# Kernel tuning notes

Measured on AMD Instinct MI355X. Metric: run time of the kernel, lower is better.

## Reference

```python
import jax, jax.numpy as jnp
import numpy as np

S, B, D_MODEL, H = 2048, 2, 1024, 16
DH = D_MODEL // H
SCALE = 1.0 / np.sqrt(DH)
NEG_INF = jnp.float32(-1e30)


def setup_inputs() -> dict:
    key = jax.random.key(0)
    ks = jax.random.split(key, 12)
    std = 1.0 / np.sqrt(D_MODEL)
    inp = {
        "query": jax.random.normal(ks[0], (S, B, D_MODEL), jnp.float32),
        "key": jax.random.normal(ks[1], (S, B, D_MODEL), jnp.float32),
        "value": jax.random.normal(ks[2], (S, B, D_MODEL), jnp.float32),
        # causal mask, shape (seq_q, seq_k, 1) per prepare_mask asserts
        "mask": jnp.tril(jnp.ones((S, S), dtype=bool))[:, :, None],
        # params stored (in, out) for x @ W
        "Wq": jax.random.normal(ks[3], (D_MODEL, H * DH), jnp.float32) * std,
        "bq": jnp.zeros((H * DH,), jnp.float32),
        "Wk": jax.random.normal(ks[4], (D_MODEL, H * DH), jnp.float32) * std,
        "bk": jnp.zeros((H * DH,), jnp.float32),
        "Wv": jax.random.normal(ks[5], (D_MODEL, H * DH), jnp.float32) * std,
        "bv": jnp.zeros((H * DH,), jnp.float32),
        "Wo": jax.random.normal(ks[6], (D_MODEL, D_MODEL), jnp.float32) * std,
        "bo": jnp.zeros((D_MODEL,), jnp.float32),
    }
    return inp


def reference(query, key, value, mask, Wq, bq, Wk, bk, Wv, bv, Wo, bo):
    seq_len, batch, _ = query.shape
    # project and split heads: (S, B, H, DH)
    q = (query @ Wq + bq).reshape(seq_len, batch, H, DH)
    k = (key @ Wk + bk).reshape(key.shape[0], batch, H, DH)
    v = (value @ Wv + bv).reshape(value.shape[0], batch, H, DH)
    # scores: (seq_q, batch, heads, seq_k)
    scores = jnp.einsum("ibhd,jbhd->ibhj", q, k) * SCALE
    # mask (seq_q, seq_k, batch_or_1) -> broadcast to (seq_q, batch, 1, seq_k)
    m = jnp.transpose(mask, (0, 2, 1))[:, :, None, :]
    scores = jnp.where(m, scores, NEG_INF)
    attn = jax.nn.softmax(scores, axis=-1)  # dropout_prob=0.0 (eval)
    x = jnp.einsum("ibhj,jbhd->ibhd", attn, v)
    x = x.reshape(seq_len, batch, H * DH)
    return x @ Wo + bo
```

## Files before the change

kernel.cpp:

```cpp
#include <hip/hip_runtime.h>
#include <hip/hip_bf16.h>
#include <cstdint>

#define S_LEN 2048
#define BATCH 2
#define DM    1024
#define NH    16
#define DH    64

typedef short s8v __attribute__((ext_vector_type(8)));
typedef float f4v __attribute__((ext_vector_type(4)));
typedef unsigned int u32x2 __attribute__((ext_vector_type(2)));

__device__ __forceinline__ ushort f2bf(float x) {
  union { float f; uint32_t u; } v; v.f = x;
  uint32_t r = v.u + 0x7fffu + ((v.u >> 16) & 1u);
  return (ushort)(r >> 16);
}
__device__ __forceinline__ float bf2f(ushort u) {
  union { uint32_t u; float f; } v; v.u = (uint32_t)u << 16; return v.f;
}
__device__ __forceinline__ uint32_t fbits(float x) {
  union { float f; uint32_t u; } v; v.f = x; return v.u;
}
__device__ __forceinline__ uint32_t bfrnd(uint32_t u) {
  return u + 0x7fffu + ((u >> 16) & 1u);
}
__device__ __forceinline__ uint32_t packbf(uint32_t flo, uint32_t fhi) {
  return __builtin_amdgcn_perm(bfrnd(fhi), bfrnd(flo), 0x07060302u);
}
__device__ __forceinline__ uint32_t packbf_tr(float lo, float hi) {
  return __builtin_amdgcn_perm(fbits(hi), fbits(lo), 0x07060302u);
}

typedef __attribute__((address_space(1))) const void gas_void;
typedef __attribute__((address_space(3))) void las_void;
__device__ __forceinline__ void gld16(void* l, const void* g) {
  __builtin_amdgcn_global_load_lds((gas_void*)(uintptr_t)g,
                                   (las_void*)(uintptr_t)l, 16, 0, 0);
}

__global__ __launch_bounds__(256)
void prep(const float* W0, const float* W1, const float* W2, const float* W3,
          ushort* T0, ushort* T1, ushort* T2, ushort* T3,
          const float* X0, const float* X1, const float* X2,
          ushort* O0, ushort* O1, ushort* O2) {
  const int z = blockIdx.z;
  if (z < 4) {
    if (blockIdx.x >= 1024) return;
    const float* W = z == 0 ? W0 : z == 1 ? W1 : z == 2 ? W2 : W3;
    ushort*      T = z == 0 ? T0 : z == 1 ? T1 : z == 2 ? T2 : T3;
    __shared__ ushort tile[32][33];
    const int n0 = (blockIdx.x & 31) * 32, k0 = (blockIdx.x >> 5) * 32;
    const int tx = threadIdx.x & 31, ty = threadIdx.x >> 5;
    #pragma unroll
    for (int r = ty; r < 32; r += 8)
      tile[r][tx] = f2bf(W[(size_t)(k0 + r) * DM + n0 + tx]);
    __syncthreads();
    #pragma unroll
    for (int r = ty; r < 32; r += 8)
      T[(size_t)(n0 + r) * DM + k0 + tx] = tile[tx][r];
  } else {
    const float* X = z == 4 ? X0 : z == 5 ? X1 : X2;
    ushort*      O = z == 4 ? O0 : z == 5 ? O1 : O2;
    const size_t i = ((size_t)blockIdx.x * 256 + threadIdx.x) * 4;
    const float4 v = *(const float4*)(X + i);
    ushort4 h;
    h.x = f2bf(v.x); h.y = f2bf(v.y); h.z = f2bf(v.z); h.w = f2bf(v.w);
    *(ushort4*)(O + i) = h;
  }
}

__global__ __launch_bounds__(512, 2)
void gemm_qkv(const ushort* __restrict__ Xq, const ushort* __restrict__ Xk,
              const ushort* __restrict__ Xv,
              const ushort* __restrict__ Wqt, const ushort* __restrict__ Wkt,
              const ushort* __restrict__ Wvt,
              const float* __restrict__ bq, const float* __restrict__ bk,
              const float* __restrict__ bv,
              ushort* __restrict__ Qh, ushort* __restrict__ Kh,
              ushort* __restrict__ Vt) {
  const int z = blockIdx.z;
  const ushort* A    = z == 0 ? Xq  : z == 1 ? Xk  : Xv;
  const ushort* Bt   = z == 0 ? Wqt : z == 1 ? Wkt : Wvt;
  const float*  bias = z == 0 ? bq  : z == 1 ? bk  : bv;

  __shared__ __align__(16) ushort lds[65536];

  const int tid = threadIdx.x, lane = tid & 63, w = tid >> 6;
  const int wm = w >> 2, wn = w & 3;
  const int lrow = lane & 15, quad = lane >> 4;
  const int m0 = blockIdx.x * 256, n0 = blockIdx.y * 256;

  const int tr = tid >> 2;
  const int swz = ((tid & 3) ^ ((tid >> 3) & 3)) * 8;
  const ushort* gA0 = A  + (size_t)(m0 + tr) * DM + swz;
  const ushort* gA1 = A  + (size_t)(m0 + 128 + tr) * DM + swz;
  const ushort* gB0 = Bt + (size_t)(n0 + tr) * DM + swz;
  const ushort* gB1 = Bt + (size_t)(n0 + 128 + tr) * DM + swz;
  const int dA0 = w * 512, dA1 = 4096 + w * 512;
  const int dB0 = 8192 + w * 512, dB1 = 12288 + w * 512;

  const int fr = (lrow >> 1) & 3;
  int pa[8], pb[4];
  #pragma unroll
  for (int i = 0; i < 8; i++)
    pa[i] = (wm * 128 + i * 16 + lrow) * 32 + ((quad ^ fr) * 8);
  #pragma unroll
  for (int j = 0; j < 4; j++)
    pb[j] = 8192 + (wn * 64 + j * 16 + lrow) * 32 + ((quad ^ fr) * 8);

  f4v acc[8][4];
  #pragma unroll
  for (int i = 0; i < 8; i++)
    #pragma unroll
    for (int j = 0; j < 4; j++)
      acc[i][j] = f4v{0.f, 0.f, 0.f, 0.f};

  #pragma unroll
  for (int t = 0; t < 3; t++) {
    const int bb = t * 16384, ko = t * 32;
    gld16(&lds[bb + dA0], gA0 + ko);
    gld16(&lds[bb + dA1], gA1 + ko);
    gld16(&lds[bb + dB0], gB0 + ko);
    gld16(&lds[bb + dB1], gB1 + ko);
  }
  asm volatile("s_waitcnt vmcnt(8)" ::: "memory");
  __builtin_amdgcn_s_barrier();

  for (int t = 0; t < 32; t++) {
    const int bb = (t & 3) * 16384;
    const bool st = t < 29;
    const int sbb = ((t + 3) & 3) * 16384;
    const int ko = (t + 3) * 32;
    s8v af[4], bf[4];
    #pragma unroll
    for (int i = 0; i < 4; i++) af[i] = *(const s8v*)&lds[bb + pa[i]];
    #pragma unroll
    for (int j = 0; j < 4; j++) bf[j] = *(const s8v*)&lds[bb + pb[j]];
    if (st) { gld16(&lds[sbb + dA0], gA0 + ko); gld16(&lds[sbb + dA1], gA1 + ko); }
    __builtin_amdgcn_s_barrier();
    __builtin_amdgcn_s_setprio(1);
    #pragma unroll
    for (int i = 0; i < 4; i++)
      #pragma unroll
      for (int j = 0; j < 4; j++)
        acc[i][j] = __builtin_amdgcn_mfma_f32_16x16x32_bf16(af[i], bf[j], acc[i][j], 0, 0, 0);
    __builtin_amdgcn_s_setprio(0);
    __builtin_amdgcn_s_barrier();
    #pragma unroll
    for (int i = 0; i < 4; i++) af[i] = *(const s8v*)&lds[bb + pa[4 + i]];
    if (st) { gld16(&lds[sbb + dB0], gB0 + ko); gld16(&lds[sbb + dB1], gB1 + ko); }
    __builtin_amdgcn_s_barrier();
    __builtin_amdgcn_s_setprio(1);
    #pragma unroll
    for (int i = 0; i < 4; i++)
      #pragma unroll
      for (int j = 0; j < 4; j++)
        acc[4 + i][j] = __builtin_amdgcn_mfma_f32_16x16x32_bf16(af[i], bf[j], acc[4 + i][j], 0, 0, 0);
    __builtin_amdgcn_s_setprio(0);
    if (t < 29)       asm volatile("s_waitcnt vmcnt(8)" ::: "memory");
    else if (t == 29) asm volatile("s_waitcnt vmcnt(4)" ::: "memory");
    else if (t == 30) asm volatile("s_waitcnt vmcnt(0)" ::: "memory");
    __builtin_amdgcn_s_barrier();
  }

  if (z <= 1) {
    ushort* O = (z == 0) ? Qh : Kh;
    #pragma unroll
    for (int i = 0; i < 8; i++)
      #pragma unroll
      for (int j = 0; j < 4; j++) {
        const int n = n0 + wn * 64 + j * 16 + lrow;
        const float bval = bias[n];
        const int h = n >> 6, d = n & 63;
        const int mb = m0 + wm * 128 + i * 16 + quad * 4;
        #pragma unroll
        for (int r = 0; r < 4; r++) {
          const int m = mb + r;
          O[((size_t)((m & 1) * NH + h) * S_LEN + (m >> 1)) * DH + d] = f2bf(acc[i][j][r] + bval);
        }
      }
  } else {
    ushort* tw = lds + w * 5120;
    const int h = (n0 + wn * 64) >> 6;
    const int s0b = (m0 + wm * 128) >> 1;
    #pragma unroll
    for (int mh = 0; mh < 2; mh++) {
      #pragma unroll
      for (int i = 0; i < 4; i++)
        #pragma unroll
        for (int j = 0; j < 4; j++) {
          const int d_l = j * 16 + lrow;
          const float bval = bias[n0 + wn * 64 + d_l];
          const f4v a = acc[mh * 4 + i][j];
          const int sbase = i * 8 + quad * 2;
          const uint32_t p0 = packbf(fbits(a[0] + bval), fbits(a[2] + bval));
          const uint32_t p1 = packbf(fbits(a[1] + bval), fbits(a[3] + bval));
          *(uint32_t*)&tw[d_l * 40 + sbase]        = p0;
          *(uint32_t*)&tw[2560 + d_l * 40 + sbase] = p1;
        }
      const int s0 = s0b + mh * 32;
      #pragma unroll
      for (int b = 0; b < 2; b++)
        #pragma unroll
        for (int p = 0; p < 4; p++) {
          const int d_l = p * 16 + (lane >> 2);
          const int c   = lane & 3;
          const s8v v = *(const s8v*)&tw[b * 2560 + d_l * 40 + c * 8];
          *(s8v*)&Vt[((size_t)(b * NH + h) * DH + d_l) * S_LEN + s0 + c * 8] = v;
        }
      if (mh == 0) __builtin_amdgcn_s_barrier();
    }
  }
}

__global__ __launch_bounds__(256)
void attn(const ushort* __restrict__ Qh, const ushort* __restrict__ Kh,
          const ushort* __restrict__ Vt, ushort* __restrict__ X,
          ushort* __restrict__ Opart, float* __restrict__ lpart) {
  __shared__ __align__(16) ushort lds[3 * 8192];

  const int tid = threadIdx.x, lane = tid & 63, w = tid >> 6;
  const int lrow = lane & 15, quad = lane >> 4;
  const int bh = blockIdx.x;
  const int slot = blockIdx.y;
  int qt, part, nparts;
  if (slot < 18)      { qt = 15 - slot / 3;        part = slot % 3;        nparts = 3; }
  else if (slot < 30) { qt = 9  - (slot - 18) / 2; part = (slot - 18) % 2; nparts = 2; }
  else                { qt = 33 - slot;            part = 0;               nparts = 1; }
  const int nj  = 2 * qt + 2;
  const int jlo = part * nj / nparts;
  const int jhi = (part + 1) * nj / nparts;
  const int iw  = qt * 128 + w * 32;

  const int srow = lane >> 3;
  const int scol = ((lane & 7) ^ srow) * 8;
  const ushort* gK0 = Kh + ((size_t)bh * S_LEN + 2 * w * 8 + srow) * DH + scol;
  const ushort* gK1 = gK0 + 8 * DH;
  const ushort* gV0 = Vt + ((size_t)bh * DH + 2 * w * 8 + srow) * S_LEN + scol;
  const ushort* gV1 = gV0 + 8 * S_LEN;
  const int lK0 = 2 * w * 512, lK1 = lK0 + 512;
  const int lV0 = 4096 + 2 * w * 512, lV1 = lV0 + 512;

  s8v aq[2][2];
  #pragma unroll
  for (int is = 0; is < 2; is++)
    #pragma unroll
    for (int kk = 0; kk < 2; kk++)
      aq[is][kk] = *(const s8v*)(Qh + ((size_t)bh * S_LEN + iw + is * 16 + lrow) * DH +
                                 kk * 32 + quad * 8);

  const int f8 = lrow & 7;
  int pk[4][2], pv[4][2];
  #pragma unroll
  for (int s4 = 0; s4 < 4; s4++)
    #pragma unroll
    for (int kk = 0; kk < 2; kk++) {
      pk[s4][kk] = (s4 * 16 + lrow) * 64 + (((kk * 4 + quad) ^ f8) * 8);
      pv[s4][kk] = 4096 + (s4 * 16 + lrow) * 64 + (((kk * 4 + quad) ^ f8) * 8);
    }

  f4v o[2][4];
  float ls[2] = {0.f, 0.f};
  #pragma unroll
  for (int is = 0; is < 2; is++)
    #pragma unroll
    for (int d4 = 0; d4 < 4; d4++) o[is][d4] = f4v{0.f, 0.f, 0.f, 0.f};

  {
    const int b0 = (jlo % 3) * 8192;
    const size_t j0 = (size_t)jlo * 64;
    gld16(&lds[b0 + lK0], gK0 + j0 * DH);
    gld16(&lds[b0 + lK1], gK1 + j0 * DH);
    gld16(&lds[b0 + lV0], gV0 + j0);
    gld16(&lds[b0 + lV1], gV1 + j0);
    if (jlo + 1 < jhi) {
      const int b1 = ((jlo + 1) % 3) * 8192;
      const size_t j1 = (size_t)(jlo + 1) * 64;
      gld16(&lds[b1 + lK0], gK0 + j1 * DH);
      gld16(&lds[b1 + lK1], gK1 + j1 * DH);
      gld16(&lds[b1 + lV0], gV0 + j1);
      gld16(&lds[b1 + lV1], gV1 + j1);
    }
  }

  int bcur = jlo % 3;
  for (int jt = jlo; jt < jhi; jt++) {
    const int j0 = jt * 64;
    if (jt + 1 < jhi) asm volatile("s_waitcnt vmcnt(4)" ::: "memory");
    else              asm volatile("s_waitcnt vmcnt(0)" ::: "memory");
    __builtin_amdgcn_s_barrier();
    const int cur = bcur * 8192;
    if (jt + 2 < jhi) {
      const int sb = (bcur == 0 ? 2 : bcur - 1) * 8192;
      const size_t jn = (size_t)(jt + 2) * 64;
      gld16(&lds[sb + lK0], gK0 + jn * DH);
      gld16(&lds[sb + lK1], gK1 + jn * DH);
      gld16(&lds[sb + lV0], gV0 + jn);
      gld16(&lds[sb + lV1], gV1 + jn);
    }
    bcur = (bcur == 2) ? 0 : bcur + 1;
    if (j0 > iw + 31) continue;

    f4v sc[2][4];
    #pragma unroll
    for (int is = 0; is < 2; is++)
      #pragma unroll
      for (int s4 = 0; s4 < 4; s4++) sc[is][s4] = f4v{0.f, 0.f, 0.f, 0.f};
    #pragma unroll
    for (int s4 = 0; s4 < 4; s4++) {
      const s8v k0f = *(const s8v*)&lds[cur + pk[s4][0]];
      const s8v k1f = *(const s8v*)&lds[cur + pk[s4][1]];
      sc[0][s4] = __builtin_amdgcn_mfma_f32_16x16x32_bf16(k0f, aq[0][0], sc[0][s4], 0, 0, 0);
      sc[1][s4] = __builtin_amdgcn_mfma_f32_16x16x32_bf16(k0f, aq[1][0], sc[1][s4], 0, 0, 0);
      sc[0][s4] = __builtin_amdgcn_mfma_f32_16x16x32_bf16(k1f, aq[0][1], sc[0][s4], 0, 0, 0);
      sc[1][s4] = __builtin_amdgcn_mfma_f32_16x16x32_bf16(k1f, aq[1][1], sc[1][s4], 0, 0, 0);
    }

    const bool needmask = (j0 + 63) > iw;
    uint32_t sw[2][4][2];
    #pragma unroll
    for (int is = 0; is < 2; is++) {
      const int ig = iw + is * 16 + lrow;
      #pragma unroll
      for (int s4 = 0; s4 < 4; s4++) {
        float e0 = __expf(sc[is][s4][0] * 0.125f);
        float e1 = __expf(sc[is][s4][1] * 0.125f);
        float e2 = __expf(sc[is][s4][2] * 0.125f);
        float e3 = __expf(sc[is][s4][3] * 0.125f);
        if (needmask) {
          const int jb = j0 + s4 * 16 + quad * 4;
          e0 = (jb + 0 > ig) ? 0.f : e0;
          e1 = (jb + 1 > ig) ? 0.f : e1;
          e2 = (jb + 2 > ig) ? 0.f : e2;
          e3 = (jb + 3 > ig) ? 0.f : e3;
        }
        ls[is] += (e0 + e1) + (e2 + e3);
        sw[is][s4][0] = packbf_tr(e0, e1);
        sw[is][s4][1] = packbf_tr(e2, e3);
      }
    }

    s8v ap[2][2];
    #pragma unroll
    for (int is = 0; is < 2; is++)
      #pragma unroll
      for (int kt = 0; kt < 2; kt++) {
        const u32x2 a32 = __builtin_amdgcn_permlane32_swap(
            sw[is][2 * kt][0], sw[is][2 * kt + 1][0], false, false);
        const u32x2 a16 = __builtin_amdgcn_permlane16_swap(a32[0], a32[1], false, false);
        const u32x2 b32 = __builtin_amdgcn_permlane32_swap(
            sw[is][2 * kt][1], sw[is][2 * kt + 1][1], false, false);
        const u32x2 b16 = __builtin_amdgcn_permlane16_swap(b32[0], b32[1], false, false);
        union { uint32_t u[4]; s8v v; } cvt;
        cvt.u[0] = a16[0]; cvt.u[1] = b16[0]; cvt.u[2] = a16[1]; cvt.u[3] = b16[1];
        ap[is][kt] = cvt.v;
      }

    #pragma unroll
    for (int d4 = 0; d4 < 4; d4++) {
      const s8v v0 = *(const s8v*)&lds[cur + pv[d4][0]];
      const s8v v1 = *(const s8v*)&lds[cur + pv[d4][1]];
      o[0][d4] = __builtin_amdgcn_mfma_f32_16x16x32_bf16(ap[0][0], v0, o[0][d4], 0, 0, 0);
      o[1][d4] = __builtin_amdgcn_mfma_f32_16x16x32_bf16(ap[1][0], v0, o[1][d4], 0, 0, 0);
      o[0][d4] = __builtin_amdgcn_mfma_f32_16x16x32_bf16(ap[0][1], v1, o[0][d4], 0, 0, 0);
      o[1][d4] = __builtin_amdgcn_mfma_f32_16x16x32_bf16(ap[1][1], v1, o[1][d4], 0, 0, 0);
    }
  }

  #pragma unroll
  for (int is = 0; is < 2; is++) {
    ls[is] += __shfl_xor(ls[is], 16, 64);
    ls[is] += __shfl_xor(ls[is], 32, 64);
  }

  if (nparts == 1) {
    const int bb = bh >> 4, h = bh & 15;
    #pragma unroll
    for (int is = 0; is < 2; is++)
      #pragma unroll
      for (int r = 0; r < 4; r++) {
        const float lv = __shfl(ls[is], quad * 16 + quad * 4 + r, 64);
        const float inv = 1.0f / lv;
        const int sg = iw + is * 16 + quad * 4 + r;
        #pragma unroll
        for (int d4 = 0; d4 < 4; d4++)
          X[((size_t)sg * BATCH + bb) * DM + h * DH + d4 * 16 + lrow] =
              f2bf(o[is][d4][r] * inv);
      }
  } else {
    ushort* Op = Opart + ((size_t)(bh * 30 + slot) * 128 + w * 32) * 64;
    #pragma unroll
    for (int is = 0; is < 2; is++)
      #pragma unroll
      for (int r = 0; r < 4; r++) {
        const int row_l = is * 16 + quad * 4 + r;
        #pragma unroll
        for (int d4 = 0; d4 < 4; d4++)
          Op[row_l * 64 + d4 * 16 + lrow] = f2bf(o[is][d4][r]);
      }
    if (quad == 0) {
      float* lp = lpart + (size_t)(bh * 30 + slot) * 128 + w * 32;
      lp[lrow]      = ls[0];
      lp[16 + lrow] = ls[1];
    }
  }
}

__global__ __launch_bounds__(256)
void combine(const ushort* __restrict__ Opart, const float* __restrict__ lpart,
             ushort* __restrict__ X) {
  const uint32_t gid = blockIdx.x * 256 + threadIdx.x;
  const int dv   = gid & 15;
  const int row  = (gid >> 4) & 127;
  const int rest = gid >> 11;
  const int qi   = rest % 12;
  const int bh   = rest / 12;
  const int qt   = 4 + qi;
  int s0, c;
  if (qt >= 10) { s0 = 3 * (15 - qt); c = 3; }
  else          { s0 = 18 + 2 * (9 - qt); c = 2; }

  float a0 = 0.f, a1 = 0.f, a2 = 0.f, a3 = 0.f, l = 0.f;
  #pragma unroll
  for (int p = 0; p < 3; p++) {
    if (p < c) {
      const size_t base = ((size_t)(bh * 30 + s0 + p) * 128 + row);
      const ushort4 v = *(const ushort4*)&Opart[base * 64 + dv * 4];
      a0 += bf2f(v.x); a1 += bf2f(v.y); a2 += bf2f(v.z); a3 += bf2f(v.w);
      l += lpart[base];
    }
  }
  const float inv = 1.0f / l;
  const int qpos = qt * 128 + row;
  const int b = bh >> 4, h = bh & 15;
  ushort4 hv;
  hv.x = f2bf(a0 * inv);
  hv.y = f2bf(a1 * inv);
  hv.z = f2bf(a2 * inv);
  hv.w = f2bf(a3 * inv);
  *(ushort4*)&X[(((size_t)qpos * BATCH + b) * NH + h) * DH + dv * 4] = hv;
}

__global__ __launch_bounds__(256)
void gemm_out(const ushort* __restrict__ A, const ushort* __restrict__ Bt,
              const float* __restrict__ bias, float* __restrict__ C) {
  __shared__ __align__(16) ushort lds[16384];

  const int tid = threadIdx.x, lane = tid & 63, w = tid >> 6;
  const int wr = w >> 1, wc = w & 1;
  const int lrow = lane & 15, quad = lane >> 4;
  const int m0 = blockIdx.x * 128, n0 = blockIdx.y * 128;

  const int sr4 = lane >> 2;
  const int scol = ((lane & 3) ^ (sr4 & 3)) * 8;

  const ushort* gA[2]; const ushort* gB[2];
  int oA[2], oB[2];
  #pragma unroll
  for (int t = 0; t < 2; t++) {
    const int c = 2 * w + t;
    gA[t] = A  + (size_t)(m0 + c * 16 + sr4) * DM + scol;
    oA[t] = c * 512;
    gB[t] = Bt + (size_t)(n0 + c * 16 + sr4) * DM + scol;
    oB[t] = 4096 + c * 512;
  }

  int pa[4], pb[4];
  #pragma unroll
  for (int i = 0; i < 4; i++) {
    pa[i] = (wr * 64 + i * 16 + lrow) * 32 + ((quad ^ (lrow & 3)) * 8);
    pb[i] = 4096 + (wc * 64 + i * 16 + lrow) * 32 + ((quad ^ (lrow & 3)) * 8);
  }

  f4v acc[4][4];
  #pragma unroll
  for (int i = 0; i < 4; i++)
    #pragma unroll
    for (int j = 0; j < 4; j++)
      acc[i][j] = f4v{0.f, 0.f, 0.f, 0.f};

  #pragma unroll
  for (int t = 0; t < 2; t++) {
    gld16(&lds[oA[t]], gA[t]);
    gld16(&lds[oB[t]], gB[t]);
  }

  for (int ks = 0; ks < 32; ks++) {
    __syncthreads();
    const int bo = (ks & 1) * 8192;
    if (ks < 31) {
      const int nb = ((ks + 1) & 1) * 8192;
      const int ko = (ks + 1) * 32;
      #pragma unroll
      for (int t = 0; t < 2; t++) {
        gld16(&lds[nb + oA[t]], gA[t] + ko);
        gld16(&lds[nb + oB[t]], gB[t] + ko);
      }
    }
    s8v af[4], bf[4];
    #pragma unroll
    for (int i = 0; i < 4; i++) af[i] = *(const s8v*)&lds[bo + pa[i]];
    #pragma unroll
    for (int j = 0; j < 4; j++) bf[j] = *(const s8v*)&lds[bo + pb[j]];
    #pragma unroll
    for (int i = 0; i < 4; i++)
      #pragma unroll
      for (int j = 0; j < 4; j++)
        acc[i][j] = __builtin_amdgcn_mfma_f32_16x16x32_bf16(af[i], bf[j], acc[i][j], 0, 0, 0);
  }

  #pragma unroll
  for (int i = 0; i < 4; i++)
    #pragma unroll
    for (int j = 0; j < 4; j++) {
      const int n = n0 + wc * 64 + j * 16 + lrow;
      const float bval = bias[n];
      const int mb = m0 + wr * 64 + i * 16 + quad * 4;
      #pragma unroll
      for (int r = 0; r < 4; r++)
        C[(size_t)(mb + r) * DM + n] = acc[i][j][r] + bval;
    }
}

extern "C" void kernel_launch(void* const* d_in, const int* in_sizes, int n_in,
                              void* d_out, int out_size, void* d_ws, size_t ws_size,
                              hipStream_t stream) {
  const float* query = (const float*)d_in[0];
  const float* key_  = (const float*)d_in[1];
  const float* value = (const float*)d_in[2];
  const float* Wq = (const float*)d_in[4];
  const float* bq = (const float*)d_in[5];
  const float* Wk = (const float*)d_in[6];
  const float* bk = (const float*)d_in[7];
  const float* Wv = (const float*)d_in[8];
  const float* bv = (const float*)d_in[9];
  const float* Wo = (const float*)d_in[10];
  const float* bo = (const float*)d_in[11];

  ushort* Wqt = (ushort*)d_ws;
  ushort* Wkt = Wqt + (size_t)1024 * 1024;
  ushort* Wvt = Wkt + (size_t)1024 * 1024;
  ushort* Wot = Wvt + (size_t)1024 * 1024;
  ushort* Xbq = Wot + (size_t)1024 * 1024;
  ushort* Xbk = Xbq + (size_t)4 * 1024 * 1024;
  ushort* Xbv = Xbk + (size_t)4 * 1024 * 1024;
  ushort* Qh  = Xbv + (size_t)4 * 1024 * 1024;
  ushort* Kh  = Qh  + (size_t)4 * 1024 * 1024;
  ushort* Vt  = Kh  + (size_t)4 * 1024 * 1024;
  ushort* Opart = Xbk;
  float*  lpart = (float*)Wqt;
  ushort* Xa  = Xbq;

  prep<<<dim3(4096, 1, 7), 256, 0, stream>>>(Wq, Wk, Wv, Wo, Wqt, Wkt, Wvt, Wot,
                                             query, key_, value, Xbq, Xbk, Xbv);
  gemm_qkv<<<dim3(16, 4, 3), 512, 0, stream>>>(Xbq, Xbk, Xbv,
                                               Wqt, Wkt, Wvt, bq, bk, bv,
                                               Qh, Kh, Vt);
  attn<<<dim3(32, 34), 256, 0, stream>>>(Qh, Kh, Vt, Xa, Opart, lpart);
  combine<<<3072, 256, 0, stream>>>(Opart, lpart, Xa);
  gemm_out<<<dim3(32, 8), 256, 0, stream>>>(Xa, Wot, bo, (float*)d_out);
}
```

Before: 229.9 us.

## Switch attention to double-buffered LDS, MFMA row sums, exp2, and setprio

The attention kernel goes from a triple-buffered K/V LDS ring with a two-tile prefetch to a double buffer with a one-tile prefetch. That cuts LDS use, which may raise occupancy, but it waits for vmcnt(0) on every iteration. Softmax denominators are now accumulated with extra MFMAs against a ones vector of bf16 probabilities, replacing the VALU adds and cross-lane shuffles. The exponential now uses exp2 with a pre-folded log2e scale, and s_setprio raises wave priority around the MFMA blocks. The denominator is now summed from bf16-rounded probabilities, so it matches the values the PV product actually uses.

```diff
diff --git a/kernel.cpp b/kernel.cpp
--- a/kernel.cpp
+++ b/kernel.cpp
@@ -219,7 +219,7 @@
 void attn(const ushort* __restrict__ Qh, const ushort* __restrict__ Kh,
           const ushort* __restrict__ Vt, ushort* __restrict__ X,
           ushort* __restrict__ Opart, float* __restrict__ lpart) {
-  __shared__ __align__(16) ushort lds[3 * 8192];
+  __shared__ __align__(16) ushort lds[2 * 8192];
 
   const int tid = threadIdx.x, lane = tid & 63, w = tid >> 6;
   const int lrow = lane & 15, quad = lane >> 4;
@@ -262,45 +262,37 @@
     }
 
   f4v o[2][4];
-  float ls[2] = {0.f, 0.f};
-  #pragma unroll
-  for (int is = 0; is < 2; is++)
+  f4v lacc[2];
+  #pragma unroll
+  for (int is = 0; is < 2; is++) {
+    lacc[is] = f4v{0.f, 0.f, 0.f, 0.f};
     #pragma unroll
     for (int d4 = 0; d4 < 4; d4++) o[is][d4] = f4v{0.f, 0.f, 0.f, 0.f};
+  }
+  const s8v vones = {0x3F80, 0x3F80, 0x3F80, 0x3F80, 0x3F80, 0x3F80, 0x3F80, 0x3F80};
 
   {
-    const int b0 = (jlo % 3) * 8192;
+    const int b0 = (jlo & 1) * 8192;
     const size_t j0 = (size_t)jlo * 64;
     gld16(&lds[b0 + lK0], gK0 + j0 * DH);
     gld16(&lds[b0 + lK1], gK1 + j0 * DH);
     gld16(&lds[b0 + lV0], gV0 + j0);
     gld16(&lds[b0 + lV1], gV1 + j0);
-    if (jlo + 1 < jhi) {
-      const int b1 = ((jlo + 1) % 3) * 8192;
-      const size_t j1 = (size_t)(jlo + 1) * 64;
-      gld16(&lds[b1 + lK0], gK0 + j1 * DH);
-      gld16(&lds[b1 + lK1], gK1 + j1 * DH);
-      gld16(&lds[b1 + lV0], gV0 + j1);
-      gld16(&lds[b1 + lV1], gV1 + j1);
-    }
-  }
-
-  int bcur = jlo % 3;
+  }
+
   for (int jt = jlo; jt < jhi; jt++) {
     const int j0 = jt * 64;
-    if (jt + 1 < jhi) asm volatile("s_waitcnt vmcnt(4)" ::: "memory");
-    else              asm volatile("s_waitcnt vmcnt(0)" ::: "memory");
+    asm volatile("s_waitcnt vmcnt(0)" ::: "memory");
     __builtin_amdgcn_s_barrier();
-    const int cur = bcur * 8192;
-    if (jt + 2 < jhi) {
-      const int sb = (bcur == 0 ? 2 : bcur - 1) * 8192;
-      const size_t jn = (size_t)(jt + 2) * 64;
-      gld16(&lds[sb + lK0], gK0 + jn * DH);
-      gld16(&lds[sb + lK1], gK1 + jn * DH);
-      gld16(&lds[sb + lV0], gV0 + jn);
-      gld16(&lds[sb + lV1], gV1 + jn);
-    }
-    bcur = (bcur == 2) ? 0 : bcur + 1;
+    const int cur = (jt & 1) * 8192;
+    if (jt + 1 < jhi) {
+      const int nb = ((jt + 1) & 1) * 8192;
+      const size_t jn = (size_t)(jt + 1) * 64;
+      gld16(&lds[nb + lK0], gK0 + jn * DH);
+      gld16(&lds[nb + lK1], gK1 + jn * DH);
+      gld16(&lds[nb + lV0], gV0 + jn);
+      gld16(&lds[nb + lV1], gV1 + jn);
+    }
     if (j0 > iw + 31) continue;
 
     f4v sc[2][4];
@@ -308,6 +300,7 @@
     for (int is = 0; is < 2; is++)
       #pragma unroll
       for (int s4 = 0; s4 < 4; s4++) sc[is][s4] = f4v{0.f, 0.f, 0.f, 0.f};
+    __builtin_amdgcn_s_setprio(1);
     #pragma unroll
     for (int s4 = 0; s4 < 4; s4++) {
       const s8v k0f = *(const s8v*)&lds[cur + pk[s4][0]];
@@ -317,18 +310,20 @@
       sc[0][s4] = __builtin_amdgcn_mfma_f32_16x16x32_bf16(k1f, aq[0][1], sc[0][s4], 0, 0, 0);
       sc[1][s4] = __builtin_amdgcn_mfma_f32_16x16x32_bf16(k1f, aq[1][1], sc[1][s4], 0, 0, 0);
     }
+    __builtin_amdgcn_s_setprio(0);
 
     const bool needmask = (j0 + 63) > iw;
+    const float C = 0.18033688011112042f;
     uint32_t sw[2][4][2];
     #pragma unroll
     for (int is = 0; is < 2; is++) {
       const int ig = iw + is * 16 + lrow;
       #pragma unroll
       for (int s4 = 0; s4 < 4; s4++) {
-        float e0 = __expf(sc[is][s4][0] * 0.125f);
-        float e1 = __expf(sc[is][s4][1] * 0.125f);
-        float e2 = __expf(sc[is][s4][2] * 0.125f);
-        float e3 = __expf(sc[is][s4][3] * 0.125f);
+        float e0 = __builtin_amdgcn_exp2f(sc[is][s4][0] * C);
+        float e1 = __builtin_amdgcn_exp2f(sc[is][s4][1] * C);
+        float e2 = __builtin_amdgcn_exp2f(sc[is][s4][2] * C);
+        float e3 = __builtin_amdgcn_exp2f(sc[is][s4][3] * C);
         if (needmask) {
           const int jb = j0 + s4 * 16 + quad * 4;
           e0 = (jb + 0 > ig) ? 0.f : e0;
@@ -336,7 +331,6 @@
           e2 = (jb + 2 > ig) ? 0.f : e2;
           e3 = (jb + 3 > ig) ? 0.f : e3;
         }
-        ls[is] += (e0 + e1) + (e2 + e3);
         sw[is][s4][0] = packbf_tr(e0, e1);
         sw[is][s4][1] = packbf_tr(e2, e3);
       }
@@ -358,6 +352,7 @@
         ap[is][kt] = cvt.v;
       }
 
+    __builtin_amdgcn_s_setprio(1);
     #pragma unroll
     for (int d4 = 0; d4 < 4; d4++) {
       const s8v v0 = *(const s8v*)&lds[cur + pv[d4][0]];
@@ -367,12 +362,11 @@
       o[0][d4] = __builtin_amdgcn_mfma_f32_16x16x32_bf16(ap[0][1], v1, o[0][d4], 0, 0, 0);
       o[1][d4] = __builtin_amdgcn_mfma_f32_16x16x32_bf16(ap[1][1], v1, o[1][d4], 0, 0, 0);
     }
-  }
-
-  #pragma unroll
-  for (int is = 0; is < 2; is++) {
-    ls[is] += __shfl_xor(ls[is], 16, 64);
-    ls[is] += __shfl_xor(ls[is], 32, 64);
+    lacc[0] = __builtin_amdgcn_mfma_f32_16x16x32_bf16(ap[0][0], vones, lacc[0], 0, 0, 0);
+    lacc[0] = __builtin_amdgcn_mfma_f32_16x16x32_bf16(ap[0][1], vones, lacc[0], 0, 0, 0);
+    lacc[1] = __builtin_amdgcn_mfma_f32_16x16x32_bf16(ap[1][0], vones, lacc[1], 0, 0, 0);
+    lacc[1] = __builtin_amdgcn_mfma_f32_16x16x32_bf16(ap[1][1], vones, lacc[1], 0, 0, 0);
+    __builtin_amdgcn_s_setprio(0);
   }
 
   if (nparts == 1) {
@@ -381,8 +375,7 @@
     for (int is = 0; is < 2; is++)
       #pragma unroll
       for (int r = 0; r < 4; r++) {
-        const float lv = __shfl(ls[is], quad * 16 + quad * 4 + r, 64);
-        const float inv = 1.0f / lv;
+        const float inv = 1.0f / lacc[is][r];
         const int sg = iw + is * 16 + quad * 4 + r;
         #pragma unroll
         for (int d4 = 0; d4 < 4; d4++)
@@ -400,10 +393,13 @@
         for (int d4 = 0; d4 < 4; d4++)
           Op[row_l * 64 + d4 * 16 + lrow] = f2bf(o[is][d4][r]);
       }
-    if (quad == 0) {
+    if (lrow == 0) {
       float* lp = lpart + (size_t)(bh * 30 + slot) * 128 + w * 32;
-      lp[lrow]      = ls[0];
-      lp[16 + lrow] = ls[1];
+      #pragma unroll
+      for (int is = 0; is < 2; is++)
+        #pragma unroll
+        for (int r = 0; r < 4; r++)
+          lp[is * 16 + quad * 4 + r] = lacc[is][r];
     }
   }
 }
```

New measurement: 225.9 us. No clear change (-1.7%).
